# Kernel optimization log

Hardware: AMD Instinct MI355X
Metric: run time of the kernel (lower is better)

Reference implementation:

```python
import jax, jax.numpy as jnp
import numpy as np

N_PER_G = 18
GRAPHS = 4096
N = GRAPHS * N_PER_G            # 73728 nodes
E = GRAPHS * N_PER_G * (N_PER_G - 1)  # 1253376 edges (fully connected per graph)
F_IN = 1536                     # sfreq * timestep
EPS = 1e-5
SLOPE = 0.01


def _lrelu(v):
    return jnp.where(v >= 0, v, SLOPE * v)


def setup_inputs() -> dict:
    key = jax.random.key(0)
    ks = jax.random.split(key, 32)
    # node features
    x = jax.random.normal(ks[0], (N, F_IN), dtype=jnp.float32)
    # fully-connected edges within each 18-node graph
    src, dst = np.meshgrid(np.arange(N_PER_G), np.arange(N_PER_G), indexing='ij')
    m = src != dst
    src, dst = src[m], dst[m]                      # [306]
    offs = (np.arange(GRAPHS) * N_PER_G)[:, None]
    row = (offs + src[None, :]).reshape(-1)
    col = (offs + dst[None, :]).reshape(-1)
    edge_index = jnp.asarray(np.stack([row, col]), dtype=jnp.int32)  # [2,E]
    edge_weight = jax.random.uniform(ks[1], (E,), dtype=jnp.float32)
    batch = jnp.asarray(np.arange(N) // N_PER_G, dtype=jnp.int32)

    def lin(k, fi, fo):
        kw, kb = jax.random.split(k)
        s = 1.0 / np.sqrt(fi)
        W = jax.random.uniform(kw, (fi, fo), jnp.float32, -s, s)
        b = jax.random.uniform(kb, (fo,), jnp.float32, -s, s)
        return W, b

    def bn(k, f):
        k1, k2 = jax.random.split(k)
        g = jnp.ones((f,), jnp.float32)
        be = jnp.zeros((f,), jnp.float32)
        rm = jax.random.normal(k1, (f,), jnp.float32) * 0.1
        rv = jax.random.uniform(k2, (f,), jnp.float32) + 0.5
        return g, be, rm, rv

    W1, b1 = lin(ks[2], F_IN, 32)
    W2, b2 = lin(ks[3], 32, 64)
    W3, b3 = lin(ks[4], 64, 128)
    g1, be1, rm1, rv1 = bn(ks[5], 32)
    g2, be2, rm2, rv2 = bn(ks[6], 64)
    g3, be3, rm3, rv3 = bn(ks[7], 128)
    fW1, fb1 = lin(ks[8], 128, 64)
    fW2, fb2 = lin(ks[9], 64, 32)
    fW3, fb3 = lin(ks[10], 32, 16)
    fW4, fb4 = lin(ks[11], 16, 1)

    return dict(x=x, edge_index=edge_index, edge_weight=edge_weight, batch=batch,
                W1=W1, b1=b1, g1=g1, be1=be1, rm1=rm1, rv1=rv1,
                W2=W2, b2=b2, g2=g2, be2=be2, rm2=rm2, rv2=rv2,
                W3=W3, b3=b3, g3=g3, be3=be3, rm3=rm3, rv3=rv3,
                fW1=fW1, fb1=fb1, fW2=fW2, fb2=fb2,
                fW3=fW3, fb3=fb3, fW4=fW4, fb4=fb4)


def _gcn_norm(edge_index, edge_weight):
    # add self loops (weight 1), symmetric normalization (PyG GCNConv, improved=False)
    row = jnp.concatenate([edge_index[0], jnp.arange(N, dtype=edge_index.dtype)])
    col = jnp.concatenate([edge_index[1], jnp.arange(N, dtype=edge_index.dtype)])
    w = jnp.concatenate([edge_weight, jnp.ones((N,), edge_weight.dtype)])
    deg = jax.ops.segment_sum(w, col, num_segments=N)
    dinv = jnp.where(deg > 0, jax.lax.rsqrt(jnp.maximum(deg, 1e-30)), 0.0)
    norm = dinv[row] * w * dinv[col]
    return row, col, norm


def _gcn(x, W, b, row, col, norm):
    h = x @ W                                       # [N, Fout]
    out = jax.ops.segment_sum(norm[:, None] * h[row], col, num_segments=N)
    return out + b


def _bn(h, g, be, rm, rv):
    return (h - rm) * jax.lax.rsqrt(rv + EPS) * g + be


def reference(x, edge_index, edge_weight, batch,
              W1, b1, g1, be1, rm1, rv1,
              W2, b2, g2, be2, rm2, rv2,
              W3, b3, g3, be3, rm3, rv3,
              fW1, fb1, fW2, fb2, fW3, fb3, fW4, fb4):
    row, col, norm = _gcn_norm(edge_index, edge_weight)
    h = _lrelu(_bn(_gcn(x, W1, b1, row, col, norm), g1, be1, rm1, rv1))
    h = _lrelu(_bn(_gcn(h, W2, b2, row, col, norm), g2, be2, rm2, rv2))
    h = _lrelu(_bn(_gcn(h, W3, b3, row, col, norm), g3, be3, rm3, rv3))
    # global mean pool over graphs
    sums = jax.ops.segment_sum(h, batch, num_segments=GRAPHS)
    cnt = jax.ops.segment_sum(jnp.ones((N,), h.dtype), batch, num_segments=GRAPHS)
    h = sums / jnp.maximum(cnt, 1.0)[:, None]       # [G,128]
    # MLP head (dropout = identity in eval)
    h = _lrelu(h @ fW1 + fb1)
    h = _lrelu(h @ fW2 + fb2)
    h = _lrelu(h @ fW3 + fb3)
    h = h @ fW4 + fb4
    return h.squeeze(-1)                            # [G]
```

## Files before the change

kernel.cpp:

```cpp
#include <hip/hip_runtime.h>
#include <stdint.h>

#define GRAPHS 4096
#define NPG 18
#define EPERG 306
#define FIN 1536
#define BN_EPS 1e-5f
#define SLOPE 0.01f
#define GPB 8
#define RPB 144

using short8  = __attribute__((ext_vector_type(8))) short;
using ushort8 = __attribute__((ext_vector_type(8))) unsigned short;
using f32x4   = __attribute__((ext_vector_type(4))) float;

__device__ __forceinline__ unsigned short f2bf(float f) {
  unsigned u = __builtin_bit_cast(unsigned, f);
  u += 0x7fffu + ((u >> 16) & 1u);
  return (unsigned short)(u >> 16);
}

__device__ __forceinline__ short8 pack_bf16(const float4& a0, const float4& a1) {
  short8 af;
  af[0] = (short)f2bf(a0.x); af[1] = (short)f2bf(a0.y);
  af[2] = (short)f2bf(a0.z); af[3] = (short)f2bf(a0.w);
  af[4] = (short)f2bf(a1.x); af[5] = (short)f2bf(a1.y);
  af[6] = (short)f2bf(a1.z); af[7] = (short)f2bf(a1.w);
  return af;
}

__device__ __forceinline__ void wave_fence() {
  asm volatile("s_waitcnt lgkmcnt(0)" ::: "memory");
}

__global__ void prep_kernel(const float* __restrict__ W1,
    const float* __restrict__ b1, const float* __restrict__ g1,
    const float* __restrict__ be1, const float* __restrict__ rm1, const float* __restrict__ rv1,
    const float* __restrict__ b2, const float* __restrict__ g2,
    const float* __restrict__ be2, const float* __restrict__ rm2, const float* __restrict__ rv2,
    const float* __restrict__ b3, const float* __restrict__ g3,
    const float* __restrict__ be3, const float* __restrict__ rm3, const float* __restrict__ rv3,
    unsigned short* __restrict__ w1frag, float* __restrict__ ab) {
  const int tid = threadIdx.x;
  if (blockIdx.x < 24) {
    int slot = blockIdx.x * 256 + tid;
    int L  = slot & 63;
    int nt = (slot >> 6) & 1;
    int ks = slot >> 7;
    int n  = nt * 16 + (L & 15);
    int kb = ks * 32 + ((L >> 4) << 3);
    ushort8 v;
#pragma unroll
    for (int j = 0; j < 8; ++j) v[j] = f2bf(W1[(kb + j) * 32 + n]);
    *((ushort8*)w1frag + slot) = v;
  } else {
    if (tid < 32) {
      float a = g1[tid] * rsqrtf(rv1[tid] + BN_EPS);
      ab[tid] = a; ab[32 + tid] = (b1[tid] - rm1[tid]) * a + be1[tid];
    }
    if (tid < 64) {
      float a = g2[tid] * rsqrtf(rv2[tid] + BN_EPS);
      ab[64 + tid] = a; ab[128 + tid] = (b2[tid] - rm2[tid]) * a + be2[tid];
    }
    if (tid < 128) {
      float a = g3[tid] * rsqrtf(rv3[tid] + BN_EPS);
      ab[192 + tid] = a; ab[320 + tid] = (b3[tid] - rm3[tid]) * a + be3[tid];
    }
  }
}

__global__ __launch_bounds__(256, 2) void gcn_fused(
    const float* __restrict__ x, const float* __restrict__ ew,
    const unsigned short* __restrict__ w1frag, const float* __restrict__ ab,
    const float* __restrict__ W2, const float* __restrict__ W3,
    const float* __restrict__ fW1, const float* __restrict__ fb1,
    const float* __restrict__ fW2, const float* __restrict__ fb2,
    const float* __restrict__ fW3, const float* __restrict__ fb3,
    const float* __restrict__ fW4, const float* __restrict__ fb4,
    float* __restrict__ out) {
  const int bid  = blockIdx.x;
  const int tid  = threadIdx.x;
  const int lane = tid & 63;
  const int wv   = tid >> 6;

  __shared__ __align__(16) float P1[RPB][36];
  __shared__ float ew_s[GPB * EPERG];
  __shared__ float dinv_s[GPB][NPG];
  __shared__ float An_s[GPB][NPG][19];
  __shared__ __align__(16) float BufA[4][NPG][68];
  __shared__ __align__(16) float BufB[4][NPG][68];

  for (int i = tid; i < GPB * EPERG; i += 256)
    ew_s[i] = ew[(size_t)bid * (GPB * EPERG) + i];

  const int arow = lane & 15;
  const int akg  = lane >> 4;
  const short8* __restrict__ wf = (const short8*)w1frag + lane;
  const float* __restrict__ xg = x + (size_t)bid * RPB * FIN;
  float* __restrict__ PT = &BufA[0][0][0];

  for (int t = wv; t < 8; t += 4) {
    f32x4 acc0 = {0.f, 0.f, 0.f, 0.f};
    f32x4 acc1 = {0.f, 0.f, 0.f, 0.f};
    const float* __restrict__ xr = xg + (size_t)(t * 16 + arow) * FIN + (akg << 3);
#pragma unroll 4
    for (int ks = 0; ks < 48; ++ks) {
      float4 a0 = *(const float4*)(xr + ks * 32);
      float4 a1 = *(const float4*)(xr + ks * 32 + 4);
      short8 af = pack_bf16(a0, a1);
      acc0 = __builtin_amdgcn_mfma_f32_16x16x32_bf16(af, wf[(ks * 2 + 0) * 64], acc0, 0, 0, 0);
      acc1 = __builtin_amdgcn_mfma_f32_16x16x32_bf16(af, wf[(ks * 2 + 1) * 64], acc1, 0, 0, 0);
    }
    const int crow = t * 16 + (akg << 2);
#pragma unroll
    for (int q = 0; q < 4; ++q) {
      P1[crow + q][arow]      = acc0[q];
      P1[crow + q][arow + 16] = acc1[q];
    }
  }
  {
    f32x4 acc0 = {0.f, 0.f, 0.f, 0.f};
    f32x4 acc1 = {0.f, 0.f, 0.f, 0.f};
    const float* __restrict__ xr = xg + (size_t)(128 + arow) * FIN + (akg << 3);
    const int k0 = wv * 12;
#pragma unroll 4
    for (int ks = k0; ks < k0 + 12; ++ks) {
      float4 a0 = *(const float4*)(xr + ks * 32);
      float4 a1 = *(const float4*)(xr + ks * 32 + 4);
      short8 af = pack_bf16(a0, a1);
      acc0 = __builtin_amdgcn_mfma_f32_16x16x32_bf16(af, wf[(ks * 2 + 0) * 64], acc0, 0, 0, 0);
      acc1 = __builtin_amdgcn_mfma_f32_16x16x32_bf16(af, wf[(ks * 2 + 1) * 64], acc1, 0, 0, 0);
    }
#pragma unroll
    for (int q = 0; q < 4; ++q) {
      PT[wv * 1224 + ((akg << 2) + q) * 32 + arow]      = acc0[q];
      PT[wv * 1224 + ((akg << 2) + q) * 32 + arow + 16] = acc1[q];
    }
  }
  __syncthreads();

  if (tid < GPB * NPG) {
    int j = tid / NPG, d = tid - j * NPG;
    const float* e = ew_s + j * EPERG;
    float deg = 1.0f;
#pragma unroll
    for (int k = 0; k < 17; ++k) {
      int s = k + (k >= d);
      deg += e[s * 17 + (d - (d > s ? 1 : 0))];
    }
    dinv_s[j][d] = rsqrtf(deg);
  }
  for (int o = tid; o < 512; o += 256) {
    int r = o >> 5, c = o & 31;
    P1[128 + r][c] = PT[o] + PT[1224 + o] + PT[2448 + o] + PT[3672 + o];
  }
  __syncthreads();

  for (int o = tid; o < GPB * NPG * NPG; o += 256) {
    int j = o / (NPG * NPG), rm = o - j * (NPG * NPG);
    int d = rm / NPG, s = rm - d * NPG;
    float v;
    if (d == s) v = dinv_s[j][d] * dinv_s[j][d];
    else        v = dinv_s[j][s] * ew_s[j * EPERG + s * 17 + (d - (d > s ? 1 : 0))] * dinv_s[j][d];
    An_s[j][d][s] = v;
  }
  __syncthreads();

  float (*A_)[68] = BufA[wv];
  float (*B_)[68] = BufB[wv];

#pragma unroll 1
  for (int jj = 0; jj < 2; ++jj) {
    const int j = wv + (jj << 2);
    const float (*An)[19] = An_s[j];
    const float* P1g = &P1[j * NPG][0];

    for (int o4 = lane; o4 < 144; o4 += 64) {
      int d = o4 >> 3, cb = (o4 & 7) << 2;
      f32x4 s = {0.f, 0.f, 0.f, 0.f};
#pragma unroll
      for (int ss = 0; ss < NPG; ++ss) {
        float a = An[d][ss];
        f32x4 p = *(const f32x4*)(P1g + ss * 36 + cb);
        s[0] = fmaf(a, p[0], s[0]); s[1] = fmaf(a, p[1], s[1]);
        s[2] = fmaf(a, p[2], s[2]); s[3] = fmaf(a, p[3], s[3]);
      }
      f32x4 al = *(const f32x4*)(ab + cb), be = *(const f32x4*)(ab + 32 + cb);
#pragma unroll
      for (int q = 0; q < 4; ++q) {
        float v = fmaf(s[q], al[q], be[q]);
        s[q] = v >= 0.f ? v : SLOPE * v;
      }
      *(f32x4*)&A_[d][cb] = s;
    }
    wave_fence();

    for (int o4 = lane; o4 < 144; o4 += 64) {
      int d = o4 >> 3, cb = (o4 & 7) << 2;
      f32x4 s = {0.f, 0.f, 0.f, 0.f};
#pragma unroll
      for (int ss = 0; ss < NPG; ++ss) {
        float a = An[d][ss];
        f32x4 p = *(const f32x4*)&A_[ss][cb];
        s[0] = fmaf(a, p[0], s[0]); s[1] = fmaf(a, p[1], s[1]);
        s[2] = fmaf(a, p[2], s[2]); s[3] = fmaf(a, p[3], s[3]);
      }
      *(f32x4*)&B_[d][cb] = s;
    }
    wave_fence();

    {
      const float al = ab[64 + lane], be = ab[128 + lane];
      float s0=0.f,s1=0.f,s2=0.f,s3=0.f,s4=0.f,s5=0.f,s6=0.f,s7=0.f,s8=0.f;
      float s9=0.f,s10=0.f,s11=0.f,s12=0.f,s13=0.f,s14=0.f,s15=0.f,s16=0.f,s17=0.f;
#define L2_ROW(i) { f32x4 g = *(const f32x4*)&B_[i][k4 * 4]; \
        s##i = fmaf(g[0], w0, fmaf(g[1], w1, fmaf(g[2], w2, fmaf(g[3], w3, s##i)))); }
      for (int k4 = 0; k4 < 8; ++k4) {
        float w0 = W2[(k4 * 4 + 0) * 64 + lane];
        float w1 = W2[(k4 * 4 + 1) * 64 + lane];
        float w2 = W2[(k4 * 4 + 2) * 64 + lane];
        float w3 = W2[(k4 * 4 + 3) * 64 + lane];
        L2_ROW(0) L2_ROW(1) L2_ROW(2) L2_ROW(3) L2_ROW(4) L2_ROW(5)
        L2_ROW(6) L2_ROW(7) L2_ROW(8) L2_ROW(9) L2_ROW(10) L2_ROW(11)
        L2_ROW(12) L2_ROW(13) L2_ROW(14) L2_ROW(15) L2_ROW(16) L2_ROW(17)
      }
#undef L2_ROW
#define L2_OUT(i) { float v = fmaf(s##i, al, be); A_[i][lane] = v >= 0.f ? v : SLOPE * v; }
      L2_OUT(0) L2_OUT(1) L2_OUT(2) L2_OUT(3) L2_OUT(4) L2_OUT(5)
      L2_OUT(6) L2_OUT(7) L2_OUT(8) L2_OUT(9) L2_OUT(10) L2_OUT(11)
      L2_OUT(12) L2_OUT(13) L2_OUT(14) L2_OUT(15) L2_OUT(16) L2_OUT(17)
#undef L2_OUT
    }
    wave_fence();

    for (int o4 = lane; o4 < 288; o4 += 64) {
      int d = o4 >> 4, cb = (o4 & 15) << 2;
      f32x4 s = {0.f, 0.f, 0.f, 0.f};
#pragma unroll
      for (int ss = 0; ss < NPG; ++ss) {
        float a = An[d][ss];
        f32x4 p = *(const f32x4*)&A_[ss][cb];
        s[0] = fmaf(a, p[0], s[0]); s[1] = fmaf(a, p[1], s[1]);
        s[2] = fmaf(a, p[2], s[2]); s[3] = fmaf(a, p[3], s[3]);
      }
      *(f32x4*)&B_[d][cb] = s;
    }
    wave_fence();

    float pool0 = 0.f, pool1 = 0.f;
#pragma unroll 1
    for (int h = 0; h < 2; ++h) {
      const int cc = (h << 6) + lane;
      const float al = ab[192 + cc], be = ab[320 + cc];
      float s0=0.f,s1=0.f,s2=0.f,s3=0.f,s4=0.f,s5=0.f,s6=0.f,s7=0.f,s8=0.f;
      float s9=0.f,s10=0.f,s11=0.f,s12=0.f,s13=0.f,s14=0.f,s15=0.f,s16=0.f,s17=0.f;
#define L3_ROW(i) { f32x4 g = *(const f32x4*)&B_[i][k4 * 4]; \
        s##i = fmaf(g[0], w0, fmaf(g[1], w1, fmaf(g[2], w2, fmaf(g[3], w3, s##i)))); }
      for (int k4 = 0; k4 < 16; ++k4) {
        float w0 = W3[(k4 * 4 + 0) * 128 + cc];
        float w1 = W3[(k4 * 4 + 1) * 128 + cc];
        float w2 = W3[(k4 * 4 + 2) * 128 + cc];
        float w3 = W3[(k4 * 4 + 3) * 128 + cc];
        L3_ROW(0) L3_ROW(1) L3_ROW(2) L3_ROW(3) L3_ROW(4) L3_ROW(5)
        L3_ROW(6) L3_ROW(7) L3_ROW(8) L3_ROW(9) L3_ROW(10) L3_ROW(11)
        L3_ROW(12) L3_ROW(13) L3_ROW(14) L3_ROW(15) L3_ROW(16) L3_ROW(17)
      }
#undef L3_ROW
      float pr = 0.f;
#define L3_POOL(i) { float v = fmaf(s##i, al, be); pr += (v >= 0.f ? v : SLOPE * v); }
      L3_POOL(0) L3_POOL(1) L3_POOL(2) L3_POOL(3) L3_POOL(4) L3_POOL(5)
      L3_POOL(6) L3_POOL(7) L3_POOL(8) L3_POOL(9) L3_POOL(10) L3_POOL(11)
      L3_POOL(12) L3_POOL(13) L3_POOL(14) L3_POOL(15) L3_POOL(16) L3_POOL(17)
#undef L3_POOL
      if (h == 0) pool0 = pr * (1.0f / 18.0f); else pool1 = pr * (1.0f / 18.0f);
    }

    float s1 = fb1[lane];
#pragma unroll
    for (int k = 0; k < 64; ++k) s1 = fmaf(__shfl(pool0, k), fW1[k * 64 + lane], s1);
#pragma unroll
    for (int k = 0; k < 64; ++k) s1 = fmaf(__shfl(pool1, k), fW1[(64 + k) * 64 + lane], s1);
    s1 = s1 >= 0.f ? s1 : SLOPE * s1;
    float s2 = fb2[lane & 31];
#pragma unroll
    for (int k = 0; k < 64; ++k) s2 = fmaf(__shfl(s1, k), fW2[k * 32 + (lane & 31)], s2);
    s2 = s2 >= 0.f ? s2 : SLOPE * s2;
    float s3 = fb3[lane & 15];
#pragma unroll
    for (int k = 0; k < 32; ++k) s3 = fmaf(__shfl(s2, k), fW3[k * 16 + (lane & 15)], s3);
    s3 = s3 >= 0.f ? s3 : SLOPE * s3;
    float s4 = fb4[0];
#pragma unroll
    for (int k = 0; k < 16; ++k) s4 = fmaf(__shfl(s3, k), fW4[k], s4);
    if (lane == 0) out[(bid << 3) + j] = s4;
  }
}

extern "C" void kernel_launch(void* const* d_in, const int* in_sizes, int n_in,
                              void* d_out, int out_size, void* d_ws, size_t ws_size,
                              hipStream_t stream) {
  const float* x   = (const float*)d_in[0];
  const float* ew  = (const float*)d_in[2];
  const float* W1  = (const float*)d_in[4];
  const float* b1  = (const float*)d_in[5];
  const float* g1  = (const float*)d_in[6];
  const float* be1 = (const float*)d_in[7];
  const float* rm1 = (const float*)d_in[8];
  const float* rv1 = (const float*)d_in[9];
  const float* W2  = (const float*)d_in[10];
  const float* b2  = (const float*)d_in[11];
  const float* g2  = (const float*)d_in[12];
  const float* be2 = (const float*)d_in[13];
  const float* rm2 = (const float*)d_in[14];
  const float* rv2 = (const float*)d_in[15];
  const float* W3  = (const float*)d_in[16];
  const float* b3  = (const float*)d_in[17];
  const float* g3  = (const float*)d_in[18];
  const float* be3 = (const float*)d_in[19];
  const float* rm3 = (const float*)d_in[20];
  const float* rv3 = (const float*)d_in[21];
  const float* fW1 = (const float*)d_in[22];
  const float* fb1 = (const float*)d_in[23];
  const float* fW2 = (const float*)d_in[24];
  const float* fb2 = (const float*)d_in[25];
  const float* fW3 = (const float*)d_in[26];
  const float* fb3 = (const float*)d_in[27];
  const float* fW4 = (const float*)d_in[28];
  const float* fb4 = (const float*)d_in[29];

  unsigned short* w1frag = (unsigned short*)d_ws;
  float* ab   = (float*)((char*)d_ws + 98304);

  prep_kernel<<<25, 256, 0, stream>>>(W1, b1, g1, be1, rm1, rv1,
                                      b2, g2, be2, rm2, rv2,
                                      b3, g3, be3, rm3, rv3,
                                      w1frag, ab);
  gcn_fused<<<512, 256, 0, stream>>>(x, ew, w1frag, ab, W2, W3, fW1,
                                     fb1, fW2, fb2, fW3, fb3, fW4, fb4,
                                     (float*)d_out);
}
```

Baseline: 849.6 us.

## Split MLP head into separate kernel and prefetch W2/W3 weights in GCN loops

Moves the MLP head out of the fused GCN kernel. Pooled features are written to workspace and a new head_kernel processes four graphs per block, staging the head weights in LDS. This frees registers and removes long serial shuffle chains from the main kernel, at the cost of an extra launch and a global round trip of the pooled data. The layer 2 and layer 3 weight loops now software-prefetch the next four weight rows, so global load latency overlaps the FMAs.

```diff
diff --git a/kernel.cpp b/kernel.cpp
--- a/kernel.cpp
+++ b/kernel.cpp
@@ -73,11 +73,7 @@
     const float* __restrict__ x, const float* __restrict__ ew,
     const unsigned short* __restrict__ w1frag, const float* __restrict__ ab,
     const float* __restrict__ W2, const float* __restrict__ W3,
-    const float* __restrict__ fW1, const float* __restrict__ fb1,
-    const float* __restrict__ fW2, const float* __restrict__ fb2,
-    const float* __restrict__ fW3, const float* __restrict__ fb3,
-    const float* __restrict__ fW4, const float* __restrict__ fb4,
-    float* __restrict__ out) {
+    float* __restrict__ pooled) {
   const int bid  = blockIdx.x;
   const int tid  = threadIdx.x;
   const int lane = tid & 63;
@@ -211,18 +207,22 @@
 
     {
       const float al = ab[64 + lane], be = ab[128 + lane];
+      float w0 = W2[0 * 64 + lane], w1 = W2[1 * 64 + lane];
+      float w2 = W2[2 * 64 + lane], w3 = W2[3 * 64 + lane];
       float s0=0.f,s1=0.f,s2=0.f,s3=0.f,s4=0.f,s5=0.f,s6=0.f,s7=0.f,s8=0.f;
       float s9=0.f,s10=0.f,s11=0.f,s12=0.f,s13=0.f,s14=0.f,s15=0.f,s16=0.f,s17=0.f;
 #define L2_ROW(i) { f32x4 g = *(const f32x4*)&B_[i][k4 * 4]; \
         s##i = fmaf(g[0], w0, fmaf(g[1], w1, fmaf(g[2], w2, fmaf(g[3], w3, s##i)))); }
       for (int k4 = 0; k4 < 8; ++k4) {
-        float w0 = W2[(k4 * 4 + 0) * 64 + lane];
-        float w1 = W2[(k4 * 4 + 1) * 64 + lane];
-        float w2 = W2[(k4 * 4 + 2) * 64 + lane];
-        float w3 = W2[(k4 * 4 + 3) * 64 + lane];
+        float n0 = 0.f, n1 = 0.f, n2 = 0.f, n3 = 0.f;
+        if (k4 < 7) {
+          n0 = W2[(k4 * 4 + 4) * 64 + lane]; n1 = W2[(k4 * 4 + 5) * 64 + lane];
+          n2 = W2[(k4 * 4 + 6) * 64 + lane]; n3 = W2[(k4 * 4 + 7) * 64 + lane];
+        }
         L2_ROW(0) L2_ROW(1) L2_ROW(2) L2_ROW(3) L2_ROW(4) L2_ROW(5)
         L2_ROW(6) L2_ROW(7) L2_ROW(8) L2_ROW(9) L2_ROW(10) L2_ROW(11)
         L2_ROW(12) L2_ROW(13) L2_ROW(14) L2_ROW(15) L2_ROW(16) L2_ROW(17)
+        w0 = n0; w1 = n1; w2 = n2; w3 = n3;
       }
 #undef L2_ROW
 #define L2_OUT(i) { float v = fmaf(s##i, al, be); A_[i][lane] = v >= 0.f ? v : SLOPE * v; }
@@ -252,18 +252,22 @@
     for (int h = 0; h < 2; ++h) {
       const int cc = (h << 6) + lane;
       const float al = ab[192 + cc], be = ab[320 + cc];
+      float w0 = W3[0 * 128 + cc], w1 = W3[1 * 128 + cc];
+      float w2 = W3[2 * 128 + cc], w3 = W3[3 * 128 + cc];
       float s0=0.f,s1=0.f,s2=0.f,s3=0.f,s4=0.f,s5=0.f,s6=0.f,s7=0.f,s8=0.f;
       float s9=0.f,s10=0.f,s11=0.f,s12=0.f,s13=0.f,s14=0.f,s15=0.f,s16=0.f,s17=0.f;
 #define L3_ROW(i) { f32x4 g = *(const f32x4*)&B_[i][k4 * 4]; \
         s##i = fmaf(g[0], w0, fmaf(g[1], w1, fmaf(g[2], w2, fmaf(g[3], w3, s##i)))); }
       for (int k4 = 0; k4 < 16; ++k4) {
-        float w0 = W3[(k4 * 4 + 0) * 128 + cc];
-        float w1 = W3[(k4 * 4 + 1) * 128 + cc];
-        float w2 = W3[(k4 * 4 + 2) * 128 + cc];
-        float w3 = W3[(k4 * 4 + 3) * 128 + cc];
+        float n0 = 0.f, n1 = 0.f, n2 = 0.f, n3 = 0.f;
+        if (k4 < 15) {
+          n0 = W3[(k4 * 4 + 4) * 128 + cc]; n1 = W3[(k4 * 4 + 5) * 128 + cc];
+          n2 = W3[(k4 * 4 + 6) * 128 + cc]; n3 = W3[(k4 * 4 + 7) * 128 + cc];
+        }
         L3_ROW(0) L3_ROW(1) L3_ROW(2) L3_ROW(3) L3_ROW(4) L3_ROW(5)
         L3_ROW(6) L3_ROW(7) L3_ROW(8) L3_ROW(9) L3_ROW(10) L3_ROW(11)
         L3_ROW(12) L3_ROW(13) L3_ROW(14) L3_ROW(15) L3_ROW(16) L3_ROW(17)
+        w0 = n0; w1 = n1; w2 = n2; w3 = n3;
       }
 #undef L3_ROW
       float pr = 0.f;
@@ -275,25 +279,59 @@
       if (h == 0) pool0 = pr * (1.0f / 18.0f); else pool1 = pr * (1.0f / 18.0f);
     }
 
-    float s1 = fb1[lane];
-#pragma unroll
-    for (int k = 0; k < 64; ++k) s1 = fmaf(__shfl(pool0, k), fW1[k * 64 + lane], s1);
-#pragma unroll
-    for (int k = 0; k < 64; ++k) s1 = fmaf(__shfl(pool1, k), fW1[(64 + k) * 64 + lane], s1);
-    s1 = s1 >= 0.f ? s1 : SLOPE * s1;
-    float s2 = fb2[lane & 31];
-#pragma unroll
-    for (int k = 0; k < 64; ++k) s2 = fmaf(__shfl(s1, k), fW2[k * 32 + (lane & 31)], s2);
-    s2 = s2 >= 0.f ? s2 : SLOPE * s2;
-    float s3 = fb3[lane & 15];
-#pragma unroll
-    for (int k = 0; k < 32; ++k) s3 = fmaf(__shfl(s2, k), fW3[k * 16 + (lane & 15)], s3);
-    s3 = s3 >= 0.f ? s3 : SLOPE * s3;
-    float s4 = fb4[0];
-#pragma unroll
-    for (int k = 0; k < 16; ++k) s4 = fmaf(__shfl(s3, k), fW4[k], s4);
-    if (lane == 0) out[(bid << 3) + j] = s4;
-  }
+    const int g = (bid << 3) + j;
+    pooled[(size_t)g * 128 + lane]      = pool0;
+    pooled[(size_t)g * 128 + 64 + lane] = pool1;
+  }
+}
+
+__global__ __launch_bounds__(256) void head_kernel(
+    const float* __restrict__ pooled,
+    const float* __restrict__ fW1, const float* __restrict__ fb1,
+    const float* __restrict__ fW2, const float* __restrict__ fb2,
+    const float* __restrict__ fW3, const float* __restrict__ fb3,
+    const float* __restrict__ fW4, const float* __restrict__ fb4,
+    float* __restrict__ out) {
+  const int tid  = threadIdx.x;
+  const int lane = tid & 63;
+  const int wv   = tid >> 6;
+
+  __shared__ __align__(16) float w1s[128 * 64];
+  __shared__ __align__(16) float w2s[64 * 32];
+  __shared__ __align__(16) float w3s[32 * 16];
+  __shared__ float w4s[16];
+
+  for (int i = tid; i < 128 * 64; i += 256) w1s[i] = fW1[i];
+  for (int i = tid; i < 64 * 32; i += 256)  w2s[i] = fW2[i];
+  for (int i = tid; i < 32 * 16; i += 256)  w3s[i] = fW3[i];
+  if (tid < 16) w4s[tid] = fW4[tid];
+  __syncthreads();
+
+  const int g = (blockIdx.x << 2) + wv;
+  const float p0 = pooled[(size_t)g * 128 + lane];
+  const float p1 = pooled[(size_t)g * 128 + 64 + lane];
+
+  float s1 = fb1[lane];
+#pragma unroll
+  for (int k = 0; k < 64; ++k) s1 = fmaf(__shfl(p0, k), w1s[k * 64 + lane], s1);
+#pragma unroll
+  for (int k = 0; k < 64; ++k) s1 = fmaf(__shfl(p1, k), w1s[(64 + k) * 64 + lane], s1);
+  s1 = s1 >= 0.f ? s1 : SLOPE * s1;
+
+  float s2 = fb2[lane & 31];
+#pragma unroll
+  for (int k = 0; k < 64; ++k) s2 = fmaf(__shfl(s1, k), w2s[k * 32 + (lane & 31)], s2);
+  s2 = s2 >= 0.f ? s2 : SLOPE * s2;
+
+  float s3 = fb3[lane & 15];
+#pragma unroll
+  for (int k = 0; k < 32; ++k) s3 = fmaf(__shfl(s2, k), w3s[k * 16 + (lane & 15)], s3);
+  s3 = s3 >= 0.f ? s3 : SLOPE * s3;
+
+  float s4 = fb4[0];
+#pragma unroll
+  for (int k = 0; k < 16; ++k) s4 = fmaf(__shfl(s3, k), w4s[k], s4);
+  if (lane == 0) out[g] = s4;
 }
 
 extern "C" void kernel_launch(void* const* d_in, const int* in_sizes, int n_in,
@@ -329,13 +367,14 @@
   const float* fb4 = (const float*)d_in[29];
 
   unsigned short* w1frag = (unsigned short*)d_ws;
-  float* ab   = (float*)((char*)d_ws + 98304);
+  float* ab     = (float*)((char*)d_ws + 98304);
+  float* pooled = (float*)((char*)d_ws + 102400);
 
   prep_kernel<<<25, 256, 0, stream>>>(W1, b1, g1, be1, rm1, rv1,
                                       b2, g2, be2, rm2, rv2,
                                       b3, g3, be3, rm3, rv3,
                                       w1frag, ab);
-  gcn_fused<<<512, 256, 0, stream>>>(x, ew, w1frag, ab, W2, W3, fW1,
-                                     fb1, fW2, fb2, fW3, fb3, fW4, fb4,
-                                     (float*)d_out);
-}
+  gcn_fused<<<512, 256, 0, stream>>>(x, ew, w1frag, ab, W2, W3, pooled);
+  head_kernel<<<1024, 256, 0, stream>>>(pooled, fW1, fb1, fW2, fb2,
+                                        fW3, fb3, fW4, fb4, (float*)d_out);
+}
```

New measurement: 717.1 us. 1.18x faster.
